# Optimization experiments

Hardware: AMD Instinct MI355X
Metric: run time of the kernel (lower is better)

## Reference

```python
import jax, jax.numpy as jnp
import numpy as np

B, S, D, H = 4, 2048, 1024, 16
DK = D // H


def setup_inputs() -> dict:
    key = jax.random.key(0)
    ks = jax.random.split(key, 7)
    scale = 0.02
    return {
        "q": jax.random.normal(ks[0], (B, S, D), jnp.float32),
        "k": jax.random.normal(ks[1], (B, S, D), jnp.float32),
        "v": jax.random.normal(ks[2], (B, S, D), jnp.float32),
        "mask": jnp.ones((B, 1, S, S), dtype=bool),
        "w_q": jax.random.normal(ks[3], (D, D), jnp.float32) * scale,
        "w_k": jax.random.normal(ks[4], (D, D), jnp.float32) * scale,
        "w_v": jax.random.normal(ks[5], (D, D), jnp.float32) * scale,
        "w_o": jax.random.normal(ks[6], (D, D), jnp.float32) * scale,
    }


def reference(q, k, v, mask, w_q, w_k, w_v, w_o):
    # Linear projections (torch nn.Linear: y = x @ W^T, bias=False)
    def split_heads(x, w):
        y = jnp.einsum('bsd,ed->bse', x, w)            # [B,S,D]
        return y.reshape(x.shape[0], x.shape[1], H, DK).transpose(0, 2, 1, 3)  # [B,H,S,DK]

    qh = split_heads(q, w_q)
    kh = split_heads(k, w_k)
    vh = split_heads(v, w_v)

    scores = jnp.einsum('bhqd,bhkd->bhqk', qh, kh) / jnp.sqrt(jnp.float32(DK))  # [B,H,S,S]
    scores = jnp.where(mask, scores, jnp.float32(-1e9))
    attn = jax.nn.softmax(scores, axis=-1)
    # dropout p=0.0 -> identity (eval mode)
    out = jnp.einsum('bhqk,bhkd->bhqd', attn, vh)      # [B,H,S,DK]
    out = out.transpose(0, 2, 1, 3).reshape(out.shape[0], out.shape[2], D)     # [B,S,D]
    return jnp.einsum('bsd,ed->bse', out, w_o)         # output projection
```

## Files before the change

kernel.cpp:

```cpp
#include <hip/hip_runtime.h>
#include <hip/hip_bf16.h>
#include <stdint.h>

typedef __bf16 bf16;
typedef __bf16 bf16x8 __attribute__((ext_vector_type(8)));
typedef float f32x4 __attribute__((ext_vector_type(4)));
typedef float f32x16 __attribute__((ext_vector_type(16)));
typedef unsigned short u16;
typedef u16 u16x8 __attribute__((ext_vector_type(8)));
typedef unsigned int u32;
typedef u32 u32x2 __attribute__((ext_vector_type(2)));
typedef u32 u32x4 __attribute__((ext_vector_type(4)));

#define GLOAD16(g, l)                                                          \
  __builtin_amdgcn_global_load_lds(                                            \
      (const __attribute__((address_space(1))) void*)(g),                      \
      (__attribute__((address_space(3))) void*)(l), 16, 0, 0)

static constexpr int BB = 4, SS = 2048, DD = 1024, HH = 16, DKH = 64;
static constexpr int NTOK = BB * SS;
static constexpr float KSC = 0.125f * 1.44269504f;

__device__ __forceinline__ u32 cvtpk_bf16(float a, float b) {
  u32 r;
  asm("v_cvt_pk_bf16_f32 %0, %1, %2" : "=v"(r) : "v"(a), "v"(b));
  return r;
}
#define PLSWAP(a, b) asm("v_permlane32_swap_b32 %0, %1" : "+v"(a), "+v"(b))

__global__ __launch_bounds__(256) void cast_w(const float* __restrict__ w0,
                                              const float* __restrict__ w1,
                                              const float* __restrict__ w2,
                                              const float* __restrict__ w3,
                                              bf16* __restrict__ dst) {
  const int bid = (int)blockIdx.x;
  const int wsel = bid >> 9;
  const int blk = bid & 511;
  const float* src = wsel == 0 ? w0 : wsel == 1 ? w1 : wsel == 2 ? w2 : w3;
  const size_t base = (size_t)blk * 2048 + (size_t)threadIdx.x * 8;
  f32x4 a = *(const f32x4*)(src + base);
  f32x4 b = *(const f32x4*)(src + base + 4);
  bf16x8 o;
#pragma unroll
  for (int j = 0; j < 4; ++j) { o[j] = (bf16)a[j]; o[j + 4] = (bf16)b[j]; }
  *(bf16x8*)(dst + (size_t)wsel * 1048576 + base) = o;
}

__global__ __launch_bounds__(256, 2) void gemm_proj(const float* __restrict__ Aq,
                                                    const float* __restrict__ Ak,
                                                    const float* __restrict__ Av_,
                                                    const bf16* __restrict__ Wb,
                                                    bf16* __restrict__ Cq,
                                                    bf16* __restrict__ Ck,
                                                    bf16* __restrict__ Cvt) {
  __shared__ __align__(16) char smem[32 * 1024];
  char* As = smem;
  char* Bs = smem + 16 * 1024;
  const int tid = threadIdx.x;
  const int lane = tid & 63;
  const int wid = tid >> 6;
  const int wr = wid >> 1, wc = wid & 1;

  const int bid0 = (int)blockIdx.x;
  const int g = bid0 >> 9;
  int bid = bid0 & 511;
  bid = (bid & 7) * 64 + (bid >> 3);

  const float* Af32;
  const bf16* Bbf;
  bf16* Cp;
  float cs = 1.0f;
  if (g == 0)      { Af32 = Aq;  Bbf = Wb;           Cp = Cq;  cs = KSC; }
  else if (g == 1) { Af32 = Ak;  Bbf = Wb + 1048576; Cp = Ck; }
  else             { Af32 = Av_; Bbf = Wb + 2097152; Cp = Cvt; }

  const int bm = (g == 2) ? (bid & 7) << 7 : (bid >> 3) << 7;
  const int bn = (g == 2) ? (bid >> 3) << 7 : (bid & 7) << 7;
  const int f32base = (g == 2) ? bn : bm;
  const int bfbase  = (g == 2) ? bm : bn;
  char* f32dst = (g == 2) ? Bs : As;
  char* bfdst  = (g == 2) ? As : Bs;
  const size_t cN = (g == 2) ? 8192 : 1024;

  const int r_ld = tid >> 3;
  const int cb_ld = (tid & 7) << 4;
  const int lrow = lane & 15;
  const int lk16 = (lane >> 4) << 4;

  f32x4 acc[4][4] = {};

  for (int kt = 0; kt < 1024; kt += 64) {
#pragma unroll
    for (int i = 0; i < 4; ++i) {
      const int row = i * 32 + r_ld;
      const float* src = Af32 + (size_t)(f32base + row) * 1024 + kt + ((tid & 7) * 8);
      f32x4 a = *(const f32x4*)src;
      f32x4 b = *(const f32x4*)(src + 4);
      bf16x8 o;
#pragma unroll
      for (int j = 0; j < 4; ++j) { o[j] = (bf16)a[j]; o[j + 4] = (bf16)b[j]; }
      *(bf16x8*)(f32dst + row * 128 + (cb_ld ^ ((row & 7) << 4))) = o;
    }
#pragma unroll
    for (int i = 0; i < 4; ++i) {
      const int row = i * 32 + r_ld;
      const int scb = cb_ld ^ ((row & 7) << 4);
      GLOAD16((const char*)(Bbf + (size_t)(bfbase + row) * 1024 + kt) + scb,
              bfdst + i * 4096 + wid * 1024);
    }
    asm volatile("s_waitcnt vmcnt(0)" ::: "memory");
    __syncthreads();
#pragma unroll
    for (int ks = 0; ks < 2; ++ks) {
      bf16x8 af[4], bfr[4];
#pragma unroll
      for (int m = 0; m < 4; ++m) {
        const int row = wr * 64 + m * 16 + lrow;
        const int cb = (ks * 64 + lk16) ^ ((row & 7) << 4);
        af[m] = *(const bf16x8*)(As + row * 128 + cb);
      }
#pragma unroll
      for (int n = 0; n < 4; ++n) {
        const int row = wc * 64 + n * 16 + lrow;
        const int cb = (ks * 64 + lk16) ^ ((row & 7) << 4);
        bfr[n] = *(const bf16x8*)(Bs + row * 128 + cb);
      }
#pragma unroll
      for (int m = 0; m < 4; ++m)
#pragma unroll
        for (int n = 0; n < 4; ++n)
          acc[m][n] = __builtin_amdgcn_mfma_f32_16x16x32_bf16(af[m], bfr[n],
                                                              acc[m][n], 0, 0, 0);
    }
    __syncthreads();
  }

#pragma unroll
  for (int m = 0; m < 4; ++m) {
    const int row0 = bm + wr * 64 + m * 16 + ((lane >> 4) << 2);
#pragma unroll
    for (int n = 0; n < 4; ++n) {
      const int col = bn + wc * 64 + n * 16 + lrow;
#pragma unroll
      for (int r = 0; r < 4; ++r)
        Cp[(size_t)(row0 + r) * cN + col] = (bf16)(acc[m][n][r] * cs);
    }
  }
}

__global__ __launch_bounds__(256, 2) void gemm_out(const bf16* __restrict__ A,
                                                   const bf16* __restrict__ W,
                                                   float* __restrict__ C) {
  __shared__ __align__(16) char smem[32 * 1024];
  char* As = smem;
  char* Bs = smem + 16 * 1024;
  const int tid = threadIdx.x;
  const int lane = tid & 63;
  const int wid = tid >> 6;
  const int wr = wid >> 1, wc = wid & 1;
  int bid = (int)blockIdx.x;
  bid = (bid & 7) * 64 + (bid >> 3);
  const int bm = (bid >> 3) << 7;
  const int bn = (bid & 7) << 7;

  const int r_ld = tid >> 3;
  const int cb_ld = (tid & 7) << 4;
  const int lrow = lane & 15;
  const int lk16 = (lane >> 4) << 4;

  f32x4 acc[4][4] = {};

  for (int kt = 0; kt < 1024; kt += 64) {
#pragma unroll
    for (int i = 0; i < 4; ++i) {
      const int row = i * 32 + r_ld;
      const int scb = cb_ld ^ ((row & 7) << 4);
      GLOAD16((const char*)(A + (size_t)(bm + row) * 1024 + kt) + scb,
              As + i * 4096 + wid * 1024);
      GLOAD16((const char*)(W + (size_t)(bn + row) * 1024 + kt) + scb,
              Bs + i * 4096 + wid * 1024);
    }
    asm volatile("s_waitcnt vmcnt(0)" ::: "memory");
    __syncthreads();
#pragma unroll
    for (int ks = 0; ks < 2; ++ks) {
      bf16x8 af[4], bfr[4];
#pragma unroll
      for (int m = 0; m < 4; ++m) {
        const int row = wr * 64 + m * 16 + lrow;
        const int cb = (ks * 64 + lk16) ^ ((row & 7) << 4);
        af[m] = *(const bf16x8*)(As + row * 128 + cb);
      }
#pragma unroll
      for (int n = 0; n < 4; ++n) {
        const int row = wc * 64 + n * 16 + lrow;
        const int cb = (ks * 64 + lk16) ^ ((row & 7) << 4);
        bfr[n] = *(const bf16x8*)(Bs + row * 128 + cb);
      }
#pragma unroll
      for (int m = 0; m < 4; ++m)
#pragma unroll
        for (int n = 0; n < 4; ++n)
          acc[m][n] = __builtin_amdgcn_mfma_f32_16x16x32_bf16(af[m], bfr[n],
                                                              acc[m][n], 0, 0, 0);
    }
    __syncthreads();
  }

#pragma unroll
  for (int m = 0; m < 4; ++m) {
    const int row0 = bm + wr * 64 + m * 16 + ((lane >> 4) << 2);
#pragma unroll
    for (int n = 0; n < 4; ++n) {
      const int col = bn + wc * 64 + n * 16 + lrow;
#pragma unroll
      for (int r = 0; r < 4; ++r)
        C[(size_t)(row0 + r) * 1024 + col] = acc[m][n][r];
    }
  }
}

__global__ __launch_bounds__(256, 4) void attn_fwd(const bf16* __restrict__ qp,
                                                   const bf16* __restrict__ kp,
                                                   const bf16* __restrict__ vt2,
                                                   bf16* __restrict__ ao) {
  __shared__ __align__(16) char smem[32 * 1024];

  const int tid = threadIdx.x;
  const int lane = tid & 63;
  const int wid = tid >> 6;
  const int l31 = lane & 31;
  const int hi = lane >> 5;
  const int hi16 = hi << 4;

  const int bid = (int)blockIdx.x;
  const int xcd = bid & 7, idx = bid >> 3;
  const int bh = xcd * 8 + (idx >> 4);
  const int qt = idx & 15;
  const int b = bh >> 4, h = bh & 15;
  const int q0 = qt << 7;

  const bf16* qrow = qp + (size_t)(b * SS + q0 + wid * 32 + l31) * DD + h * DKH;
  bf16x8 qf[4];
#pragma unroll
  for (int st = 0; st < 4; ++st)
    qf[st] = *(const bf16x8*)(qrow + st * 16 + hi * 8);

  f32x16 o[2] = {};
  float l = 0.f;

  const char* ksrc = (const char*)(kp + (size_t)b * SS * DD + h * DKH);
  const char* vsrc = (const char*)vt2 + (size_t)h * 64 * 16384 + (size_t)b * 4096;
  const int srow = tid >> 3;
  const int scol16 = (tid & 7) << 4;

#define STAGE(KV0, BUFB)                                                       \
  {                                                                            \
    _Pragma("unroll") for (int i = 0; i < 2; ++i) {                            \
      const int row = i * 32 + srow;                                           \
      const int sc = scol16 ^ ((row & 7) << 4);                                \
      GLOAD16(ksrc + (size_t)((KV0) + row) * 2048 + sc,                        \
              smem + (BUFB) + i * 4096 + wid * 1024);                          \
      GLOAD16(vsrc + (size_t)row * 16384 + (size_t)(KV0) * 2 + sc,             \
              smem + (BUFB) + 8192 + i * 4096 + wid * 1024);                   \
    }                                                                          \
  }

  STAGE(0, 0);
  asm volatile("s_waitcnt vmcnt(0)" ::: "memory");
  __syncthreads();

  const int NT = SS / 64;
  for (int t = 0; t < NT; ++t) {
    const int cur = (t & 1) * 16384;
    if (t + 1 < NT) STAGE((t + 1) * 64, cur ^ 16384);

    const char* Kb = smem + cur;
    const char* Vb = Kb + 8192;

    f32x16 s[2] = {};
    __builtin_amdgcn_s_setprio(1);
#pragma unroll
    for (int st = 0; st < 4; ++st)
#pragma unroll
      for (int sub = 0; sub < 2; ++sub) {
        const int row = sub * 32 + l31;
        bf16x8 kf = *(const bf16x8*)(Kb + row * 128 +
                                     ((st * 32 + hi16) ^ ((row & 7) << 4)));
        s[sub] = __builtin_amdgcn_mfma_f32_32x32x16_bf16(kf, qf[st], s[sub],
                                                         0, 0, 0);
      }
    __builtin_amdgcn_s_setprio(0);

#pragma unroll
    for (int sub = 0; sub < 2; ++sub)
#pragma unroll
      for (int r = 0; r < 16; ++r) s[sub][r] = exp2f(s[sub][r]);

    float red[16];
#pragma unroll
    for (int r = 0; r < 16; ++r) red[r] = s[0][r] + s[1][r];
#pragma unroll
    for (int stp = 8; stp >= 1; stp >>= 1)
#pragma unroll
      for (int i = 0; i < 8; ++i)
        if (i < stp) red[i] += red[i + stp];
    float rs = red[0];
    rs += __shfl_xor(rs, 32);
    l += rs;

    bf16x8 pa[4];
#pragma unroll
    for (int ks = 0; ks < 4; ++ks) {
      const int sub = ks >> 1, bse = (ks & 1) * 8;
      u32 a0 = cvtpk_bf16(s[sub][bse + 0], s[sub][bse + 1]);
      u32 b0 = cvtpk_bf16(s[sub][bse + 4], s[sub][bse + 5]);
      PLSWAP(a0, b0);
      u32 a1 = cvtpk_bf16(s[sub][bse + 2], s[sub][bse + 3]);
      u32 b1 = cvtpk_bf16(s[sub][bse + 6], s[sub][bse + 7]);
      PLSWAP(a1, b1);
      union { u32x4 w; bf16x8 v; } u;
      u.w[0] = a0; u.w[1] = a1; u.w[2] = b0; u.w[3] = b1;
      pa[ks] = u.v;
    }

    __builtin_amdgcn_s_setprio(1);
#pragma unroll
    for (int da = 0; da < 2; ++da)
#pragma unroll
      for (int ks = 0; ks < 4; ++ks) {
        const int row = da * 32 + l31;
        bf16x8 vf = *(const bf16x8*)(Vb + row * 128 +
                                     ((ks * 32 + hi16) ^ ((row & 7) << 4)));
        o[da] = __builtin_amdgcn_mfma_f32_32x32x16_bf16(vf, pa[ks], o[da],
                                                        0, 0, 0);
      }
    __builtin_amdgcn_s_setprio(0);

    asm volatile("s_waitcnt vmcnt(0)" ::: "memory");
    __syncthreads();
  }

  char* ow = smem + wid * 4096;
  {
    const float inv = 1.0f / l;
    const int q = l31;
    const int swz = (q & 7) << 4;
#pragma unroll
    for (int da = 0; da < 2; ++da)
#pragma unroll
      for (int g = 0; g < 4; ++g) {
        u32x2 pr;
        pr[0] = cvtpk_bf16(o[da][g * 4 + 0] * inv, o[da][g * 4 + 1] * inv);
        pr[1] = cvtpk_bf16(o[da][g * 4 + 2] * inv, o[da][g * 4 + 3] * inv);
        *(u32x2*)(ow + q * 128 + ((da * 64 + g * 16 + hi * 8) ^ swz)) = pr;
      }
  }
  __syncthreads();
#pragma unroll
  for (int p = 0; p < 4; ++p) {
    const int qb = p * 32 + (tid >> 3);
    const int w = qb >> 5, ql = qb & 31;
    bf16x8 v = *(const bf16x8*)(smem + w * 4096 + ql * 128 +
                                (((tid & 7) << 4) ^ ((ql & 7) << 4)));
    *(bf16x8*)(ao + (size_t)(b * SS + q0 + qb) * DD + h * DKH + (tid & 7) * 8) = v;
  }
#undef STAGE
}

extern "C" void kernel_launch(void* const* d_in, const int* in_sizes, int n_in,
                              void* d_out, int out_size, void* d_ws,
                              size_t ws_size, hipStream_t stream) {
  const float* q  = (const float*)d_in[0];
  const float* k  = (const float*)d_in[1];
  const float* v  = (const float*)d_in[2];
  const float* wq = (const float*)d_in[4];
  const float* wk = (const float*)d_in[5];
  const float* wv = (const float*)d_in[6];
  const float* wo = (const float*)d_in[7];
  float* out = (float*)d_out;

  const size_t T = (size_t)NTOK * DD;
  bf16* wb  = (bf16*)d_ws;
  bf16* qp  = wb + 4 * 1048576;
  bf16* kp  = qp + T;
  bf16* vt2 = kp + T;
  bf16* ao  = vt2 + T;

  dim3 blk(256);
  cast_w<<<dim3(2048), blk, 0, stream>>>(wq, wk, wv, wo, wb);
  gemm_proj<<<dim3(1536), blk, 0, stream>>>(q, k, v, wb, qp, kp, vt2);
  attn_fwd<<<dim3(1024), blk, 0, stream>>>(qp, kp, vt2, ao);
  gemm_out<<<dim3(512), blk, 0, stream>>>(ao, wb + 3145728, out);
}
```

Before: 189.5 us.

## Split attention KV tile across waves and halve query tile per block

The attention kernel now processes 64 query rows per block instead of 128, with each pair of waves splitting the 64-key tile into two 32-key halves (split-K within a block). Partial outputs and row sums from the second half are combined through shared memory before normalization, and the grid doubles to 2048 blocks. Launch-bound occupancy hints are raised for both the projection GEMM and attention kernels. This aims to increase parallelism and occupancy, at the cost of doubling K/V staging traffic per query and adding a cross-wave reduction.

```diff
diff --git a/kernel.cpp b/kernel.cpp
--- a/kernel.cpp
+++ b/kernel.cpp
@@ -46,7 +46,7 @@
   *(bf16x8*)(dst + (size_t)wsel * 1048576 + base) = o;
 }
 
-__global__ __launch_bounds__(256, 2) void gemm_proj(const float* __restrict__ Aq,
+__global__ __launch_bounds__(256, 3) void gemm_proj(const float* __restrict__ Aq,
                                                     const float* __restrict__ Ak,
                                                     const float* __restrict__ Av_,
                                                     const bf16* __restrict__ Wb,
@@ -220,7 +220,7 @@
   }
 }
 
-__global__ __launch_bounds__(256, 4) void attn_fwd(const bf16* __restrict__ qp,
+__global__ __launch_bounds__(256, 5) void attn_fwd(const bf16* __restrict__ qp,
                                                    const bf16* __restrict__ kp,
                                                    const bf16* __restrict__ vt2,
                                                    bf16* __restrict__ ao) {
@@ -229,18 +229,20 @@
   const int tid = threadIdx.x;
   const int lane = tid & 63;
   const int wid = tid >> 6;
+  const int qs = wid & 1;
+  const int kvs = wid >> 1;
   const int l31 = lane & 31;
   const int hi = lane >> 5;
   const int hi16 = hi << 4;
 
   const int bid = (int)blockIdx.x;
   const int xcd = bid & 7, idx = bid >> 3;
-  const int bh = xcd * 8 + (idx >> 4);
-  const int qt = idx & 15;
+  const int bh = xcd * 8 + (idx >> 5);
+  const int qt = idx & 31;
   const int b = bh >> 4, h = bh & 15;
-  const int q0 = qt << 7;
-
-  const bf16* qrow = qp + (size_t)(b * SS + q0 + wid * 32 + l31) * DD + h * DKH;
+  const int q0 = qt << 6;
+
+  const bf16* qrow = qp + (size_t)(b * SS + q0 + qs * 32 + l31) * DD + h * DKH;
   bf16x8 qf[4];
 #pragma unroll
   for (int st = 0; st < 4; ++st)
@@ -278,46 +280,41 @@
     const char* Kb = smem + cur;
     const char* Vb = Kb + 8192;
 
-    f32x16 s[2] = {};
+    f32x16 s = {};
     __builtin_amdgcn_s_setprio(1);
 #pragma unroll
-    for (int st = 0; st < 4; ++st)
-#pragma unroll
-      for (int sub = 0; sub < 2; ++sub) {
-        const int row = sub * 32 + l31;
-        bf16x8 kf = *(const bf16x8*)(Kb + row * 128 +
-                                     ((st * 32 + hi16) ^ ((row & 7) << 4)));
-        s[sub] = __builtin_amdgcn_mfma_f32_32x32x16_bf16(kf, qf[st], s[sub],
-                                                         0, 0, 0);
-      }
+    for (int st = 0; st < 4; ++st) {
+      const int row = kvs * 32 + l31;
+      bf16x8 kf = *(const bf16x8*)(Kb + row * 128 +
+                                   ((st * 32 + hi16) ^ ((row & 7) << 4)));
+      s = __builtin_amdgcn_mfma_f32_32x32x16_bf16(kf, qf[st], s, 0, 0, 0);
+    }
     __builtin_amdgcn_s_setprio(0);
 
 #pragma unroll
-    for (int sub = 0; sub < 2; ++sub)
-#pragma unroll
-      for (int r = 0; r < 16; ++r) s[sub][r] = exp2f(s[sub][r]);
-
-    float red[16];
-#pragma unroll
-    for (int r = 0; r < 16; ++r) red[r] = s[0][r] + s[1][r];
-#pragma unroll
-    for (int stp = 8; stp >= 1; stp >>= 1)
-#pragma unroll
-      for (int i = 0; i < 8; ++i)
+    for (int r = 0; r < 16; ++r) s[r] = exp2f(s[r]);
+
+    float red[8];
+#pragma unroll
+    for (int i = 0; i < 8; ++i) red[i] = s[i] + s[i + 8];
+#pragma unroll
+    for (int stp = 4; stp >= 1; stp >>= 1)
+#pragma unroll
+      for (int i = 0; i < 4; ++i)
         if (i < stp) red[i] += red[i + stp];
     float rs = red[0];
     rs += __shfl_xor(rs, 32);
     l += rs;
 
-    bf16x8 pa[4];
-#pragma unroll
-    for (int ks = 0; ks < 4; ++ks) {
-      const int sub = ks >> 1, bse = (ks & 1) * 8;
-      u32 a0 = cvtpk_bf16(s[sub][bse + 0], s[sub][bse + 1]);
-      u32 b0 = cvtpk_bf16(s[sub][bse + 4], s[sub][bse + 5]);
+    bf16x8 pa[2];
+#pragma unroll
+    for (int ks = 0; ks < 2; ++ks) {
+      const int bse = ks * 8;
+      u32 a0 = cvtpk_bf16(s[bse + 0], s[bse + 1]);
+      u32 b0 = cvtpk_bf16(s[bse + 4], s[bse + 5]);
       PLSWAP(a0, b0);
-      u32 a1 = cvtpk_bf16(s[sub][bse + 2], s[sub][bse + 3]);
-      u32 b1 = cvtpk_bf16(s[sub][bse + 6], s[sub][bse + 7]);
+      u32 a1 = cvtpk_bf16(s[bse + 2], s[bse + 3]);
+      u32 b1 = cvtpk_bf16(s[bse + 6], s[bse + 7]);
       PLSWAP(a1, b1);
       union { u32x4 w; bf16x8 v; } u;
       u.w[0] = a0; u.w[1] = a1; u.w[2] = b0; u.w[3] = b1;
@@ -328,10 +325,10 @@
 #pragma unroll
     for (int da = 0; da < 2; ++da)
 #pragma unroll
-      for (int ks = 0; ks < 4; ++ks) {
+      for (int ks = 0; ks < 2; ++ks) {
         const int row = da * 32 + l31;
         bf16x8 vf = *(const bf16x8*)(Vb + row * 128 +
-                                     ((ks * 32 + hi16) ^ ((row & 7) << 4)));
+                                     ((kvs * 64 + ks * 32 + hi16) ^ ((row & 7) << 4)));
         o[da] = __builtin_amdgcn_mfma_f32_32x32x16_bf16(vf, pa[ks], o[da],
                                                         0, 0, 0);
       }
@@ -341,24 +338,53 @@
     __syncthreads();
   }
 
-  char* ow = smem + wid * 4096;
-  {
-    const float inv = 1.0f / l;
+  if (kvs == 1) {
+    char* pr = smem + 16384 + qs * 8192 + lane * 128;
+#pragma unroll
+    for (int da = 0; da < 2; ++da)
+#pragma unroll
+      for (int g2 = 0; g2 < 4; ++g2) {
+        f32x4 t;
+#pragma unroll
+        for (int j = 0; j < 4; ++j) t[j] = o[da][g2 * 4 + j];
+        *(f32x4*)(pr + da * 64 + ((g2 ^ (lane & 3)) << 4)) = t;
+      }
+    if (lane < 32) *(float*)(smem + qs * 128 + lane * 4) = l;
+  }
+  __syncthreads();
+  float inv = 0.f;
+  if (kvs == 0) {
+    const char* pr = smem + 16384 + qs * 8192 + lane * 128;
+#pragma unroll
+    for (int da = 0; da < 2; ++da)
+#pragma unroll
+      for (int g2 = 0; g2 < 4; ++g2) {
+        f32x4 t = *(const f32x4*)(pr + da * 64 + ((g2 ^ (lane & 3)) << 4));
+#pragma unroll
+        for (int j = 0; j < 4; ++j) o[da][g2 * 4 + j] += t[j];
+      }
+    l += *(const float*)(smem + qs * 128 + l31 * 4);
+    inv = 1.0f / l;
+  }
+  __syncthreads();
+
+  if (kvs == 0) {
+    char* ow = smem + qs * 4096;
     const int q = l31;
     const int swz = (q & 7) << 4;
 #pragma unroll
     for (int da = 0; da < 2; ++da)
 #pragma unroll
-      for (int g = 0; g < 4; ++g) {
-        u32x2 pr;
-        pr[0] = cvtpk_bf16(o[da][g * 4 + 0] * inv, o[da][g * 4 + 1] * inv);
-        pr[1] = cvtpk_bf16(o[da][g * 4 + 2] * inv, o[da][g * 4 + 3] * inv);
-        *(u32x2*)(ow + q * 128 + ((da * 64 + g * 16 + hi * 8) ^ swz)) = pr;
+      for (int g2 = 0; g2 < 4; ++g2) {
+        u32x2 pr2;
+        pr2[0] = cvtpk_bf16(o[da][g2 * 4 + 0] * inv, o[da][g2 * 4 + 1] * inv);
+        pr2[1] = cvtpk_bf16(o[da][g2 * 4 + 2] * inv, o[da][g2 * 4 + 3] * inv);
+        *(u32x2*)(ow + q * 128 + ((da * 64 + g2 * 16 + hi * 8) ^ swz)) = pr2;
       }
   }
   __syncthreads();
 #pragma unroll
-  for (int p = 0; p < 4; ++p) {
+  for (int p = 0; p < 2; ++p) {
     const int qb = p * 32 + (tid >> 3);
     const int w = qb >> 5, ql = qb & 31;
     bf16x8 v = *(const bf16x8*)(smem + w * 4096 + ql * 128 +
@@ -390,6 +416,6 @@
   dim3 blk(256);
   cast_w<<<dim3(2048), blk, 0, stream>>>(wq, wk, wv, wo, wb);
   gemm_proj<<<dim3(1536), blk, 0, stream>>>(q, k, v, wb, qp, kp, vt2);
-  attn_fwd<<<dim3(1024), blk, 0, stream>>>(qp, kp, vt2, ao);
+  attn_fwd<<<dim3(2048), blk, 0, stream>>>(qp, kp, vt2, ao);
   gemm_out<<<dim3(512), blk, 0, stream>>>(ao, wb + 3145728, out);
 }
```

Result: slower. 200.8 us (+6.0%).
